# Kernel optimization log

Hardware: AMD Instinct MI355X
Metric: run time of the kernel (lower is better)

## Reference

```python
import jax, jax.numpy as jnp
import numpy as np
from jax import lax


def _sobel_weights():
    kx = np.array([[[1, 0, -1], [1, 0, -1], [1, 0, -1]],
                   [[2, 0, -2], [2, 0, -2], [2, 0, -2]],
                   [[1, 0, -1], [1, 0, -1], [1, 0, -1]]], dtype=np.float32)
    ky = np.array([[[1, 2, 1], [1, 2, 1], [1, 2, 1]],
                   [[0, 0, 0], [0, 0, 0], [0, 0, 0]],
                   [[-1, -2, -1], [-1, -2, -1], [-1, -2, -1]]], dtype=np.float32)
    kz = np.array([[[1, 2, 1], [0, 0, 0], [-1, -2, -1]],
                   [[1, 2, 1], [0, 0, 0], [-1, -2, -1]],
                   [[1, 2, 1], [0, 0, 0], [-1, -2, -1]]], dtype=np.float32)
    # [O=3, I=1, 3, 3, 3]: all three directional stencils in a single conv
    return jnp.asarray(np.stack([kx, ky, kz])[:, None])


def setup_inputs() -> dict:
    key = jax.random.key(0)
    data = jax.random.uniform(key, (4, 1, 256, 256, 64), dtype=jnp.float32)
    return {"data": data, "weight": _sobel_weights()}


def reference(data, weight):
    # data: [B,1,D,H,W]; weight: [3,1,3,3,3]
    x = jnp.where(data == 255.0, 0.0, data)
    # torch Conv3d is cross-correlation, matching lax.conv_general_dilated
    grad = lax.conv_general_dilated(
        x, weight, window_strides=(1, 1, 1), padding="SAME",
        dimension_numbers=("NCDHW", "OIDHW", "NCDHW"))  # [B,3,D,H,W]
    # dx/dy/dz thresholding: any nonzero gradient becomes 1 (else stays 0)
    b = (jnp.abs(grad) > 0).astype(x.dtype)
    # channel-wise L2 norm of binarized gradients, then threshold at 1
    norm = jnp.sqrt(jnp.sum(b * b, axis=1, keepdims=True))  # [B,1,D,H,W]
    return (norm > 1.0).astype(x.dtype)
```

## Files before the change

kernel.cpp:

```cpp
#include <hip/hip_runtime.h>


constexpr int DDIM = 256;
constexpr int HDIM = 256;
constexpr int WWID = 64;
constexpr int DC   = 4;
constexpr int HT   = 8;

struct P3 { float ds[4], ss[4], sd[4]; };

__device__ __forceinline__ float dpp_up1(float v) {
  return __builtin_bit_cast(float, __builtin_amdgcn_update_dpp(
      0, __builtin_bit_cast(int, v), 0x111, 0xf, 0xf, true));
}
__device__ __forceinline__ float dpp_dn1(float v) {
  return __builtin_bit_cast(float, __builtin_amdgcn_update_dpp(
      0, __builtin_bit_cast(int, v), 0x101, 0xf, 0xf, true));
}

__global__ __launch_bounds__(128) void sobel3d_kernel(
    const float* __restrict__ in, float* __restrict__ out) {
  const int lane = threadIdx.x;
  const int wg   = lane & 15;
  const int hs   = lane >> 4;
  const int w0   = wg * 4;
  const int h    = blockIdx.x * HT + threadIdx.y * 4 + hs;
  const int d0   = blockIdx.y * DC;
  const int b    = blockIdx.z;

  const size_t plane = (size_t)HDIM * WWID;
  const float* src = in  + (size_t)b * DDIM * plane;
  float*       dst = out + (size_t)b * DDIM * plane;

  const size_t offb = (size_t)h * WWID + w0;
  const bool va = (h > 0);
  const bool vc = (h + 1 < HDIM);

  auto loadPlane = [&](int d, float4& ra, float4& rb, float4& rc) {
    if ((unsigned)d < (unsigned)DDIM) {
      const float* p = src + (size_t)d * plane;
      rb = *(const float4*)(p + offb);
      ra = va ? *(const float4*)(p + offb - WWID) : float4{0.f, 0.f, 0.f, 0.f};
      rc = vc ? *(const float4*)(p + offb + WWID) : float4{0.f, 0.f, 0.f, 0.f};
    } else {
      ra = rb = rc = float4{0.f, 0.f, 0.f, 0.f};
    }
  };

  auto rowSD = [&](float4 v, float* S, float* D) {
    const float x1 = (v.x == 255.f) ? 0.f : v.x;
    const float x2 = (v.y == 255.f) ? 0.f : v.y;
    const float x3 = (v.z == 255.f) ? 0.f : v.z;
    const float x4 = (v.w == 255.f) ? 0.f : v.w;
    const float xm = dpp_up1(x4);
    const float xp = dpp_dn1(x1);
    const float x[6] = {xm, x1, x2, x3, x4, xp};
    #pragma unroll
    for (int i = 0; i < 4; ++i) {
      S[i] = fmaf(2.f, x[i + 1], x[i]) + x[i + 2];
      D[i] = x[i] - x[i + 2];
    }
  };

  auto partials = [&](const float4& ra, const float4& rb, const float4& rc, P3& o) {
    float Sa[4], Da[4], Sb[4], Db[4], Sc[4], Dc[4];
    rowSD(ra, Sa, Da);
    rowSD(rb, Sb, Db);
    rowSD(rc, Sc, Dc);
    #pragma unroll
    for (int i = 0; i < 4; ++i) {
      o.ds[i] = Da[i] + Db[i] + Dc[i];
      o.ss[i] = Sa[i] + Sb[i] + Sc[i];
      o.sd[i] = Sa[i] - Sc[i];
    }
  };

  auto emit = [&](int d, const P3& p, const P3& c, const P3& n) {
    float4 o;
    #pragma unroll
    for (int i = 0; i < 4; ++i) {
      const float Gx = fmaf(2.f, c.ds[i], p.ds[i]) + n.ds[i];
      const float Gy = p.ss[i] - n.ss[i];
      const float Gz = p.sd[i] + c.sd[i] + n.sd[i];
      const int cnt = (Gx != 0.f) + (Gy != 0.f) + (Gz != 0.f);
      (&o.x)[i] = (cnt >= 2) ? 1.f : 0.f;
    }
    *(float4*)(dst + (size_t)d * plane + offb) = o;
  };

  float4 A0, B0, C0, A1, B1, C1, A2, B2, C2;
  P3 p0, p1, p2;

  loadPlane(d0 - 1, A0, B0, C0);
  loadPlane(d0,     A1, B1, C1);
  loadPlane(d0 + 1, A2, B2, C2);
  partials(A0, B0, C0, p0);  loadPlane(d0 + 2, A0, B0, C0);
  partials(A1, B1, C1, p1);  loadPlane(d0 + 3, A1, B1, C1);
  partials(A2, B2, C2, p2);  loadPlane(d0 + 4, A2, B2, C2);
  emit(d0,     p0, p1, p2);
  partials(A0, B0, C0, p0);
  emit(d0 + 1, p1, p2, p0);
  partials(A1, B1, C1, p1);
  emit(d0 + 2, p2, p0, p1);
  partials(A2, B2, C2, p2);
  emit(d0 + 3, p0, p1, p2);
}

extern "C" void kernel_launch(void* const* d_in, const int* in_sizes, int n_in,
                              void* d_out, int out_size, void* d_ws, size_t ws_size,
                              hipStream_t stream) {
  const float* data = (const float*)d_in[0];
  float* out = (float*)d_out;
  dim3 grid(HDIM / HT, DDIM / DC, 4);
  dim3 block(WWID, 2);
  sobel3d_kernel<<<grid, block, 0, stream>>>(data, out);
}
```

Before: 30.30 us.

## Deepen depth pipeline to eight planes with four-buffer prefetch and nontemporal stores

```diff
diff --git a/kernel.cpp b/kernel.cpp
--- a/kernel.cpp
+++ b/kernel.cpp
@@ -4,10 +4,13 @@
 constexpr int DDIM = 256;
 constexpr int HDIM = 256;
 constexpr int WWID = 64;
-constexpr int DC   = 4;
+constexpr int DC   = 8;
 constexpr int HT   = 8;
 
-struct P3 { float ds[4], ss[4], sd[4]; };
+typedef float vfloat4 __attribute__((ext_vector_type(4)));
+
+struct P3  { float ds[4], ss[4], sd[4]; };
+struct Raw { float4 a, b, c; };
 
 __device__ __forceinline__ float dpp_up1(float v) {
   return __builtin_bit_cast(float, __builtin_amdgcn_update_dpp(
@@ -36,14 +39,14 @@
   const bool va = (h > 0);
   const bool vc = (h + 1 < HDIM);
 
-  auto loadPlane = [&](int d, float4& ra, float4& rb, float4& rc) {
+  auto loadPlane = [&](int d, Raw& r) {
     if ((unsigned)d < (unsigned)DDIM) {
       const float* p = src + (size_t)d * plane;
-      rb = *(const float4*)(p + offb);
-      ra = va ? *(const float4*)(p + offb - WWID) : float4{0.f, 0.f, 0.f, 0.f};
-      rc = vc ? *(const float4*)(p + offb + WWID) : float4{0.f, 0.f, 0.f, 0.f};
+      r.b = *(const float4*)(p + offb);
+      r.a = va ? *(const float4*)(p + offb - WWID) : float4{0.f, 0.f, 0.f, 0.f};
+      r.c = vc ? *(const float4*)(p + offb + WWID) : float4{0.f, 0.f, 0.f, 0.f};
     } else {
-      ra = rb = rc = float4{0.f, 0.f, 0.f, 0.f};
+      r.a = r.b = r.c = float4{0.f, 0.f, 0.f, 0.f};
     }
   };
 
@@ -62,11 +65,11 @@
     }
   };
 
-  auto partials = [&](const float4& ra, const float4& rb, const float4& rc, P3& o) {
+  auto partials = [&](const Raw& r, P3& o) {
     float Sa[4], Da[4], Sb[4], Db[4], Sc[4], Dc[4];
-    rowSD(ra, Sa, Da);
-    rowSD(rb, Sb, Db);
-    rowSD(rc, Sc, Dc);
+    rowSD(r.a, Sa, Da);
+    rowSD(r.b, Sb, Db);
+    rowSD(r.c, Sc, Dc);
     #pragma unroll
     for (int i = 0; i < 4; ++i) {
       o.ds[i] = Da[i] + Db[i] + Dc[i];
@@ -76,34 +79,35 @@
   };
 
   auto emit = [&](int d, const P3& p, const P3& c, const P3& n) {
-    float4 o;
+    vfloat4 o;
     #pragma unroll
     for (int i = 0; i < 4; ++i) {
       const float Gx = fmaf(2.f, c.ds[i], p.ds[i]) + n.ds[i];
       const float Gy = p.ss[i] - n.ss[i];
       const float Gz = p.sd[i] + c.sd[i] + n.sd[i];
       const int cnt = (Gx != 0.f) + (Gy != 0.f) + (Gz != 0.f);
-      (&o.x)[i] = (cnt >= 2) ? 1.f : 0.f;
+      o[i] = (cnt >= 2) ? 1.f : 0.f;
     }
-    *(float4*)(dst + (size_t)d * plane + offb) = o;
+    __builtin_nontemporal_store(o, (vfloat4*)(dst + (size_t)d * plane + offb));
   };
 
-  float4 A0, B0, C0, A1, B1, C1, A2, B2, C2;
+  Raw A, B, C, D;
   P3 p0, p1, p2;
 
-  loadPlane(d0 - 1, A0, B0, C0);
-  loadPlane(d0,     A1, B1, C1);
-  loadPlane(d0 + 1, A2, B2, C2);
-  partials(A0, B0, C0, p0);  loadPlane(d0 + 2, A0, B0, C0);
-  partials(A1, B1, C1, p1);  loadPlane(d0 + 3, A1, B1, C1);
-  partials(A2, B2, C2, p2);  loadPlane(d0 + 4, A2, B2, C2);
-  emit(d0,     p0, p1, p2);
-  partials(A0, B0, C0, p0);
-  emit(d0 + 1, p1, p2, p0);
-  partials(A1, B1, C1, p1);
-  emit(d0 + 2, p2, p0, p1);
-  partials(A2, B2, C2, p2);
-  emit(d0 + 3, p0, p1, p2);
+  loadPlane(d0 - 1, A);
+  loadPlane(d0,     B);
+  loadPlane(d0 + 1, C);
+  loadPlane(d0 + 2, D);
+  partials(A, p0);  loadPlane(d0 + 3, A);
+  partials(B, p1);  loadPlane(d0 + 4, B);
+  partials(C, p2);  emit(d0,     p0, p1, p2);  loadPlane(d0 + 5, C);
+  partials(D, p0);  emit(d0 + 1, p1, p2, p0);  loadPlane(d0 + 6, D);
+  partials(A, p1);  emit(d0 + 2, p2, p0, p1);  loadPlane(d0 + 7, A);
+  partials(B, p2);  emit(d0 + 3, p0, p1, p2);  loadPlane(d0 + 8, B);
+  partials(C, p0);  emit(d0 + 4, p1, p2, p0);
+  partials(D, p1);  emit(d0 + 5, p2, p0, p1);
+  partials(A, p2);  emit(d0 + 6, p0, p1, p2);
+  partials(B, p0);  emit(d0 + 7, p1, p2, p0);
 }
 
 extern "C" void kernel_launch(void* const* d_in, const int* in_sizes, int n_in,
```

Result: slower. 32.30 us (+6.6%).
